# Performance work log

Hardware: AMD Instinct MI355X
Metric: run time of the kernel (lower is better)

## Reference

```python
import jax, jax.numpy as jnp
import numpy as np

B, N, H, E = 64, 512, 32, 4
N_STEPS = 5
ANNO = 1


def setup_inputs() -> dict:
    key = jax.random.key(0)
    ks = jax.random.split(key, 20)
    sc_h = 1.0 / np.sqrt(H)
    sc_3h = 1.0 / np.sqrt(3 * H)
    sc_ha = 1.0 / np.sqrt(H + ANNO)
    inp = {
        "x": jax.random.normal(ks[0], (B, N, H), jnp.float32),
        "a": jax.random.uniform(ks[1], (B, N, ANNO), jnp.float32),
        "m": jax.random.uniform(ks[2], (B, N, 2 * N * E), jnp.float32),
        # fc_in / fc_out: hidden -> hidden*n_edge (torch Linear: W [out,in])
        "W_in": jax.random.normal(ks[3], (H * E, H), jnp.float32) * sc_h,
        "b_in": jax.random.normal(ks[4], (H * E,), jnp.float32) * sc_h,
        "W_out": jax.random.normal(ks[5], (H * E, H), jnp.float32) * sc_h,
        "b_out": jax.random.normal(ks[6], (H * E,), jnp.float32) * sc_h,
        # GRU-style gates: 3*hidden -> hidden
        "Wz": jax.random.normal(ks[7], (H, 3 * H), jnp.float32) * sc_3h,
        "bz": jax.random.normal(ks[8], (H,), jnp.float32) * sc_3h,
        "Wr": jax.random.normal(ks[9], (H, 3 * H), jnp.float32) * sc_3h,
        "br": jax.random.normal(ks[10], (H,), jnp.float32) * sc_3h,
        "Wt": jax.random.normal(ks[11], (H, 3 * H), jnp.float32) * sc_3h,
        "bt": jax.random.normal(ks[12], (H,), jnp.float32) * sc_3h,
        # output head (task_id not in {18,19}): fc1, fc2
        "W1": jax.random.normal(ks[13], (H, H + ANNO), jnp.float32) * sc_ha,
        "b1": jax.random.normal(ks[14], (H,), jnp.float32) * sc_ha,
        "W2": jax.random.normal(ks[15], (1, H), jnp.float32) * sc_h,
        "b2": jax.random.normal(ks[16], (1,), jnp.float32) * sc_h,
    }
    return inp


def _reorder(s):
    # [B, N, H*E] -> view(B,N,H,E) -> transpose(2,3) -> transpose(1,2) -> [B, E*N, H]
    return s.reshape(B, N, H, E).transpose(0, 3, 1, 2).reshape(B, E * N, H)


def reference(x, a, m, W_in, b_in, W_out, b_out, Wz, bz, Wr, br, Wt, bt, W1, b1, W2, b2):
    m_in = m[:, :, : N * E]   # [B, N, N*E]
    m_out = m[:, :, N * E :]  # [B, N, N*E]
    h = x
    for _ in range(N_STEPS):
        s_in = _reorder(h @ W_in.T + b_in)    # [B, E*N, H]
        s_out = _reorder(h @ W_out.T + b_out)  # [B, E*N, H]
        a_in = jnp.einsum("bnm,bmh->bnh", m_in, s_in)
        a_out = jnp.einsum("bnm,bmh->bnh", m_out, s_out)
        cat = jnp.concatenate([a_in, a_out, h], axis=-1)  # [B, N, 3H]
        z = jax.nn.sigmoid(cat @ Wz.T + bz)
        r = jax.nn.sigmoid(cat @ Wr.T + br)
        joint = jnp.concatenate([a_in, a_out, r * h], axis=-1)
        h_hat = jnp.tanh(joint @ Wt.T + bt)
        h = (1.0 - z) * h + z * h_hat
    out = jnp.tanh(jnp.concatenate([h, a], axis=-1) @ W1.T + b1)  # [B, N, H]
    out = (out @ W2.T + b2).sum(-1)  # [B, N]
    return out
```

## Files before the change

kernel.cpp:

```cpp
#include <hip/hip_runtime.h>
#include <hip/hip_fp16.h>
#include <math.h>

#define B_ 64
#define N_ 512
#define H_ 32
#define E_ 4
#define NSTEPS 5
#define KTOT 2048

typedef _Float16 half8 __attribute__((ext_vector_type(8)));
typedef float   f32x4 __attribute__((ext_vector_type(4)));

__device__ __forceinline__ void gld16(const void* g, void* l) {
    __builtin_amdgcn_global_load_lds(
        (const __attribute__((address_space(1))) void*)g,
        (__attribute__((address_space(3))) void*)l, 16, 0, 0);
}

__global__ __launch_bounds__(256) void k_init_h(const float* __restrict__ x,
                                                float* __restrict__ h) {
    int i = blockIdx.x * blockDim.x + threadIdx.x;
    ((f32x4*)h)[i] = ((const f32x4*)x)[i];
}

__global__ __launch_bounds__(256) void k_s(const float* __restrict__ hstate,
                                           const float* __restrict__ W_in,
                                           const float* __restrict__ b_in,
                                           const float* __restrict__ W_out,
                                           const float* __restrict__ b_out,
                                           _Float16* __restrict__ sT_in_hi,
                                           _Float16* __restrict__ sT_in_lo,
                                           _Float16* __restrict__ sT_out_hi,
                                           _Float16* __restrict__ sT_out_lo) {
    int b  = blockIdx.x >> 3;
    int n0 = (blockIdx.x & 7) * 64;
    int lane = threadIdx.x & 63;
    int w = __builtin_amdgcn_readfirstlane((int)(threadIdx.x >> 6));
    int n = n0 + lane;

    const float* hrow = hstate + ((size_t)b * N_ + n) * H_;
    f32x4 hv[8];
#pragma unroll
    for (int c = 0; c < 8; c++) hv[c] = ((const f32x4*)hrow)[c];

#pragma unroll 4
    for (int o = 0; o < 32; o++) {
        int he = w * 32 + o;
        const f32x4* wr = (const f32x4*)(W_in + (size_t)he * H_);
        float acc = b_in[he];
#pragma unroll
        for (int c = 0; c < 8; c++) {
            f32x4 wv = wr[c];
            acc += hv[c][0]*wv[0] + hv[c][1]*wv[1] + hv[c][2]*wv[2] + hv[c][3]*wv[3];
        }
        int hh = he >> 2, e = he & 3;
        size_t idx = ((size_t)b * H_ + hh) * KTOT + e * N_ + n;
        _Float16 hi = (_Float16)acc;
        sT_in_hi[idx] = hi;
        sT_in_lo[idx] = (_Float16)(acc - (float)hi);
    }
#pragma unroll 4
    for (int o = 0; o < 32; o++) {
        int he = w * 32 + o;
        const f32x4* wr = (const f32x4*)(W_out + (size_t)he * H_);
        float acc = b_out[he];
#pragma unroll
        for (int c = 0; c < 8; c++) {
            f32x4 wv = wr[c];
            acc += hv[c][0]*wv[0] + hv[c][1]*wv[1] + hv[c][2]*wv[2] + hv[c][3]*wv[3];
        }
        int hh = he >> 2, e = he & 3;
        size_t idx = ((size_t)b * H_ + hh) * KTOT + e * N_ + n;
        _Float16 hi = (_Float16)acc;
        sT_out_hi[idx] = hi;
        sT_out_lo[idx] = (_Float16)(acc - (float)hi);
    }
}

#define CHB   256
#define BUFA2 16384
#define BUFB2 8192
#define BUFSZ 24576
#define NCH   32
__global__ __launch_bounds__(256, 2) void k_einsum_p3(const float* __restrict__ m,
                                                      const _Float16* __restrict__ sT_in_hi,
                                                      const _Float16* __restrict__ sT_in_lo,
                                                      const _Float16* __restrict__ sT_out_hi,
                                                      const _Float16* __restrict__ sT_out_lo,
                                                      float* __restrict__ a_in,
                                                      float* __restrict__ a_out) {
    __shared__ __align__(16) char lds[3 * BUFSZ];
    int bid  = blockIdx.x;
    int xcd  = bid & 7, loc = bid >> 3;
    int pair = xcd * 16 + (loc >> 3);
    int nblk = loc & 7;
    int b    = pair >> 1;
    int dir  = pair & 1;
    int n0   = nblk * 64;
    int tid  = threadIdx.x;
    int w    = tid >> 6;
    int lane = tid & 63;
    int l15  = lane & 15;
    int quad = lane >> 4;

    const char* mBase = (const char*)(m + ((size_t)(b * N_ + n0)) * (2 * KTOT)
                                        + (size_t)dir * KTOT);
    const _Float16* sHi = (dir ? sT_out_hi : sT_in_hi) + (size_t)b * H_ * KTOT;
    const _Float16* sLo = (dir ? sT_out_lo : sT_in_lo) + (size_t)b * H_ * KTOT;
    float* aout = dir ? a_out : a_in;

    int bp   = w >> 1;
    int brb  = (w & 1) << 4;
    const char* sP = (const char*)(bp ? sLo : sHi);

    auto STAGE = [&](int c, int buf) {
        char* dA = lds + buf * BUFSZ;
        char* dB = lds + buf * BUFSZ + BUFA2 + bp * 4096;
#pragma unroll
        for (int i = 0; i < 4; i++) {
            int r = (w << 4) + i * 4 + (lane >> 4);
            const char* g = mBase + (size_t)r * (2 * KTOT * 4) + c * CHB
                            + (((lane & 15) * 16) ^ ((r & 7) << 4));
            gld16(g, dA + ((w << 4) + i * 4) * 256);
        }
#pragma unroll
        for (int i = 0; i < 2; i++) {
            int r = brb + i * 8 + (lane >> 3);
            const char* g = sP + (size_t)r * (KTOT * 2) + c * 128
                            + (((lane & 7) * 16) ^ ((r & 7) << 4));
            gld16(g, dB + (brb + i * 8) * 128);
        }
    };

    f32x4 acc0 = {0.f,0.f,0.f,0.f}, acc1 = {0.f,0.f,0.f,0.f};

    int rowA  = (w << 4) + l15;
    int swzA  = (rowA & 7) << 4;
    int swzB0 = (l15 & 7) << 4;

    STAGE(0, 0);
    STAGE(1, 1);

    for (int c = 0; c < NCH; c++) {
        int buf = c % 3;
        if (c + 2 < NCH) STAGE(c + 2, (c + 2) % 3);
        if (c + 2 < NCH)      asm volatile("s_waitcnt vmcnt(12)" ::: "memory");
        else if (c + 1 < NCH) asm volatile("s_waitcnt vmcnt(6)"  ::: "memory");
        else                  asm volatile("s_waitcnt vmcnt(0)"  ::: "memory");
        __builtin_amdgcn_s_barrier();
        __builtin_amdgcn_sched_barrier(0);

        const char* Ab = lds + buf * BUFSZ + rowA * 256;
        const char* Bh = lds + buf * BUFSZ + BUFA2;
        const char* Bl = Bh + 4096;
#pragma unroll
        for (int it = 0; it < 2; it++) {
            int kab = it * 128 + quad * 32;
            f32x4 a0 = *(const f32x4*)(Ab + (kab ^ swzA));
            f32x4 a1 = *(const f32x4*)(Ab + ((kab + 16) ^ swzA));

            int kbb = it * 64 + quad * 16;
            int o0 = l15 * 128        + (kbb ^ swzB0);
            int o1 = (l15 + 16) * 128 + (kbb ^ swzB0);
            half8 Bhi0 = *(const half8*)(Bh + o0);
            half8 Bhi1 = *(const half8*)(Bh + o1);
            half8 Blo0 = *(const half8*)(Bl + o0);
            half8 Blo1 = *(const half8*)(Bl + o1);

            half8 Ahi, Alo;
#pragma unroll
            for (int j = 0; j < 4; j++) {
                float v0 = a0[j], v1 = a1[j];
                _Float16 h0 = (_Float16)v0, h1 = (_Float16)v1;
                Ahi[j]     = h0;
                Ahi[j + 4] = h1;
                Alo[j]     = (_Float16)(v0 - (float)h0);
                Alo[j + 4] = (_Float16)(v1 - (float)h1);
            }
            acc0 = __builtin_amdgcn_mfma_f32_16x16x32_f16(Ahi, Bhi0, acc0, 0, 0, 0);
            acc1 = __builtin_amdgcn_mfma_f32_16x16x32_f16(Ahi, Bhi1, acc1, 0, 0, 0);
            acc0 = __builtin_amdgcn_mfma_f32_16x16x32_f16(Ahi, Blo0, acc0, 0, 0, 0);
            acc1 = __builtin_amdgcn_mfma_f32_16x16x32_f16(Ahi, Blo1, acc1, 0, 0, 0);
            acc0 = __builtin_amdgcn_mfma_f32_16x16x32_f16(Alo, Bhi0, acc0, 0, 0, 0);
            acc1 = __builtin_amdgcn_mfma_f32_16x16x32_f16(Alo, Bhi1, acc1, 0, 0, 0);
        }
        __builtin_amdgcn_sched_barrier(0);
        __builtin_amdgcn_s_barrier();
    }

#pragma unroll
    for (int r = 0; r < 4; r++) {
        size_t rr = (size_t)b * N_ + (n0 + w * 16 + quad * 4 + r);
        aout[rr * H_ + l15]      = acc0[r];
        aout[rr * H_ + 16 + l15] = acc1[r];
    }
}

__global__ __launch_bounds__(256) void k_gate(const float* __restrict__ a_in,
                                              const float* __restrict__ a_out,
                                              float* __restrict__ hstate,
                                              const float* __restrict__ Wz,
                                              const float* __restrict__ bz,
                                              const float* __restrict__ Wr,
                                              const float* __restrict__ br,
                                              const float* __restrict__ Wt,
                                              const float* __restrict__ bt) {
    __shared__ float cat[8][96];
    __shared__ float rh[8][32];
    int base = blockIdx.x * 8;
    int t = threadIdx.x;

    for (int idx = t; idx < 768; idx += 256) {
        int r = idx / 96, c = idx - r * 96;
        size_t row = (size_t)(base + r);
        float v;
        if (c < 32)      v = a_in [row * 32 + c];
        else if (c < 64) v = a_out[row * 32 + (c - 32)];
        else             v = hstate[row * 32 + (c - 64)];
        cat[r][c] = v;
    }
    __syncthreads();

    int r = t >> 5, i = t & 31;
    float az = bz[i], ar = br[i];
    const f32x4* wzr = (const f32x4*)(Wz + (size_t)i * 96);
    const f32x4* wrr = (const f32x4*)(Wr + (size_t)i * 96);
    const f32x4* crow = (const f32x4*)cat[r];
#pragma unroll
    for (int kc = 0; kc < 24; kc++) {
        f32x4 cv = crow[kc];
        f32x4 wz = wzr[kc];
        f32x4 wr = wrr[kc];
        az += cv[0]*wz[0] + cv[1]*wz[1] + cv[2]*wz[2] + cv[3]*wz[3];
        ar += cv[0]*wr[0] + cv[1]*wr[1] + cv[2]*wr[2] + cv[3]*wr[3];
    }
    float z  = 1.f / (1.f + __expf(-az));
    float rg = 1.f / (1.f + __expf(-ar));
    float hold = cat[r][64 + i];
    rh[r][i] = rg * hold;
    __syncthreads();

    float at = bt[i];
    const f32x4* wtr = (const f32x4*)(Wt + (size_t)i * 96);
#pragma unroll
    for (int kc = 0; kc < 16; kc++) {
        f32x4 cv = crow[kc];
        f32x4 wt = wtr[kc];
        at += cv[0]*wt[0] + cv[1]*wt[1] + cv[2]*wt[2] + cv[3]*wt[3];
    }
    const f32x4* rrow = (const f32x4*)rh[r];
#pragma unroll
    for (int kc = 0; kc < 8; kc++) {
        f32x4 cv = rrow[kc];
        f32x4 wt = wtr[16 + kc];
        at += cv[0]*wt[0] + cv[1]*wt[1] + cv[2]*wt[2] + cv[3]*wt[3];
    }
    float hh = tanhf(at);
    hstate[(size_t)(base + r) * 32 + i] = (1.f - z) * hold + z * hh;
}

__global__ __launch_bounds__(256) void k_final(const float* __restrict__ hstate,
                                               const float* __restrict__ a,
                                               const float* __restrict__ W1,
                                               const float* __restrict__ b1,
                                               const float* __restrict__ W2,
                                               const float* __restrict__ b2,
                                               float* __restrict__ out) {
    __shared__ float hl[8][32];
    __shared__ float as[8];
    int base = blockIdx.x * 8;
    int t = threadIdx.x;
    {
        int r = t >> 5, c = t & 31;
        hl[r][c] = hstate[(size_t)(base + r) * 32 + c];
        if (t < 8) as[t] = a[base + t];
    }
    __syncthreads();
    int r = t >> 5, j = t & 31;
    float acc = b1[j];
    const float* w1r = W1 + (size_t)j * 33;
#pragma unroll
    for (int i2 = 0; i2 < 32; i2++) acc += hl[r][i2] * w1r[i2];
    acc += as[r] * w1r[32];
    float o = tanhf(acc) * W2[j];
#pragma unroll
    for (int off = 16; off; off >>= 1) o += __shfl_xor(o, off, 32);
    if (j == 0) out[base + r] = o + b2[0];
}

extern "C" void kernel_launch(void* const* d_in, const int* in_sizes, int n_in,
                              void* d_out, int out_size, void* d_ws, size_t ws_size,
                              hipStream_t stream) {
    const float* x     = (const float*)d_in[0];
    const float* a     = (const float*)d_in[1];
    const float* m     = (const float*)d_in[2];
    const float* W_in  = (const float*)d_in[3];
    const float* b_in  = (const float*)d_in[4];
    const float* W_out = (const float*)d_in[5];
    const float* b_out = (const float*)d_in[6];
    const float* Wz    = (const float*)d_in[7];
    const float* bz    = (const float*)d_in[8];
    const float* Wr    = (const float*)d_in[9];
    const float* br    = (const float*)d_in[10];
    const float* Wt    = (const float*)d_in[11];
    const float* bt    = (const float*)d_in[12];
    const float* W1    = (const float*)d_in[13];
    const float* b1    = (const float*)d_in[14];
    const float* W2    = (const float*)d_in[15];
    const float* b2    = (const float*)d_in[16];
    float* out = (float*)d_out;

    char* ws = (char*)d_ws;
    float*    h         = (float*)(ws);
    float*    a_in      = (float*)(ws + ((size_t)4  << 20));
    float*    a_out     = (float*)(ws + ((size_t)8  << 20));
    _Float16* sT_in_hi  = (_Float16*)(ws + ((size_t)12 << 20));
    _Float16* sT_in_lo  = (_Float16*)(ws + ((size_t)20 << 20));
    _Float16* sT_out_hi = (_Float16*)(ws + ((size_t)28 << 20));
    _Float16* sT_out_lo = (_Float16*)(ws + ((size_t)36 << 20));

    k_init_h<<<1024, 256, 0, stream>>>(x, h);
    for (int s = 0; s < NSTEPS; s++) {
        k_s<<<512, 256, 0, stream>>>(h, W_in, b_in, W_out, b_out,
                                     sT_in_hi, sT_in_lo, sT_out_hi, sT_out_lo);
        k_einsum_p3<<<1024, 256, 0, stream>>>(m, sT_in_hi, sT_in_lo,
                                              sT_out_hi, sT_out_lo,
                                              a_in, a_out);
        k_gate<<<4096, 256, 0, stream>>>(a_in, a_out, h, Wz, bz, Wr, br, Wt, bt);
    }
    k_final<<<4096, 256, 0, stream>>>(h, a, W1, b1, W2, b2, out);
}
```

Baseline: 2.176 ms.

## Fuse einsum and GRU gate into one kernel, drop init copy

Merges the two einsum directions and the gate computation into a single kernel. Each block handles both in and out directions for its 64 rows, keeping a_in/a_out in LDS instead of writing them to global memory. The initial h copy is removed by reading x directly on the first step. The grid halves from 1024 to 512 blocks, each doing twice the streaming work. Pipelining drops from triple to double buffering, which may expose more memory latency on the dominant m stream.

```diff
diff --git a/kernel.cpp b/kernel.cpp
--- a/kernel.cpp
+++ b/kernel.cpp
@@ -18,13 +18,7 @@
         (__attribute__((address_space(3))) void*)l, 16, 0, 0);
 }
 
-__global__ __launch_bounds__(256) void k_init_h(const float* __restrict__ x,
-                                                float* __restrict__ h) {
-    int i = blockIdx.x * blockDim.x + threadIdx.x;
-    ((f32x4*)h)[i] = ((const f32x4*)x)[i];
-}
-
-__global__ __launch_bounds__(256) void k_s(const float* __restrict__ hstate,
+__global__ __launch_bounds__(256) void k_s(const float* __restrict__ hsrc,
                                            const float* __restrict__ W_in,
                                            const float* __restrict__ b_in,
                                            const float* __restrict__ W_out,
@@ -39,7 +33,7 @@
     int w = __builtin_amdgcn_readfirstlane((int)(threadIdx.x >> 6));
     int n = n0 + lane;
 
-    const float* hrow = hstate + ((size_t)b * N_ + n) * H_;
+    const float* hrow = hsrc + ((size_t)b * N_ + n) * H_;
     f32x4 hv[8];
 #pragma unroll
     for (int c = 0; c < 8; c++) hv[c] = ((const f32x4*)hrow)[c];
@@ -80,23 +74,27 @@
 
 #define CHB   256
 #define BUFA2 16384
-#define BUFB2 8192
 #define BUFSZ 24576
-#define NCH   32
-__global__ __launch_bounds__(256, 2) void k_einsum_p3(const float* __restrict__ m,
-                                                      const _Float16* __restrict__ sT_in_hi,
-                                                      const _Float16* __restrict__ sT_in_lo,
-                                                      const _Float16* __restrict__ sT_out_hi,
-                                                      const _Float16* __restrict__ sT_out_lo,
-                                                      float* __restrict__ a_in,
-                                                      float* __restrict__ a_out) {
-    __shared__ __align__(16) char lds[3 * BUFSZ];
+__global__ __launch_bounds__(256, 2) void k_fuse(const float* __restrict__ m,
+                                                 const _Float16* __restrict__ sT_in_hi,
+                                                 const _Float16* __restrict__ sT_in_lo,
+                                                 const _Float16* __restrict__ sT_out_hi,
+                                                 const _Float16* __restrict__ sT_out_lo,
+                                                 const float* __restrict__ hold_src,
+                                                 float* __restrict__ hstate,
+                                                 const float* __restrict__ Wz,
+                                                 const float* __restrict__ bz,
+                                                 const float* __restrict__ Wr,
+                                                 const float* __restrict__ br,
+                                                 const float* __restrict__ Wt,
+                                                 const float* __restrict__ bt) {
+    __shared__ __align__(16) char lds[2 * BUFSZ];
+    __shared__ float aBuf[64][96];
+    __shared__ float rhL[8][32];
     int bid  = blockIdx.x;
     int xcd  = bid & 7, loc = bid >> 3;
-    int pair = xcd * 16 + (loc >> 3);
+    int b    = xcd * 8 + (loc >> 3);
     int nblk = loc & 7;
-    int b    = pair >> 1;
-    int dir  = pair & 1;
     int n0   = nblk * 64;
     int tid  = threadIdx.x;
     int w    = tid >> 6;
@@ -104,23 +102,29 @@
     int l15  = lane & 15;
     int quad = lane >> 4;
 
-    const char* mBase = (const char*)(m + ((size_t)(b * N_ + n0)) * (2 * KTOT)
-                                        + (size_t)dir * KTOT);
-    const _Float16* sHi = (dir ? sT_out_hi : sT_in_hi) + (size_t)b * H_ * KTOT;
-    const _Float16* sLo = (dir ? sT_out_lo : sT_in_lo) + (size_t)b * H_ * KTOT;
-    float* aout = dir ? a_out : a_in;
+    const char* mBase = (const char*)(m + ((size_t)(b * N_ + n0)) * (2 * KTOT));
+    const float* hold = hold_src + ((size_t)b * N_ + n0) * H_;
+
+    for (int i = tid; i < 2048; i += 256)
+        aBuf[i >> 5][64 + (i & 31)] = hold[((i >> 5) * 32) + (i & 31)];
 
     int bp   = w >> 1;
     int brb  = (w & 1) << 4;
-    const char* sP = (const char*)(bp ? sLo : sHi);
-
-    auto STAGE = [&](int c, int buf) {
+    const char* sHiD[2] = { (const char*)(sT_in_hi  + (size_t)b * H_ * KTOT),
+                            (const char*)(sT_out_hi + (size_t)b * H_ * KTOT) };
+    const char* sLoD[2] = { (const char*)(sT_in_lo  + (size_t)b * H_ * KTOT),
+                            (const char*)(sT_out_lo + (size_t)b * H_ * KTOT) };
+
+    auto STAGE = [&](int cc, int buf) {
+        int dir_s = cc >> 5, c = cc & 31;
         char* dA = lds + buf * BUFSZ;
         char* dB = lds + buf * BUFSZ + BUFA2 + bp * 4096;
+        const char* mD = mBase + dir_s * 8192;
+        const char* sP = bp ? sLoD[dir_s] : sHiD[dir_s];
 #pragma unroll
         for (int i = 0; i < 4; i++) {
             int r = (w << 4) + i * 4 + (lane >> 4);
-            const char* g = mBase + (size_t)r * (2 * KTOT * 4) + c * CHB
+            const char* g = mD + (size_t)r * (2 * KTOT * 4) + c * CHB
                             + (((lane & 15) * 16) ^ ((r & 7) << 4));
             gld16(g, dA + ((w << 4) + i * 4) * 256);
         }
@@ -140,14 +144,12 @@
     int swzB0 = (l15 & 7) << 4;
 
     STAGE(0, 0);
-    STAGE(1, 1);
-
-    for (int c = 0; c < NCH; c++) {
-        int buf = c % 3;
-        if (c + 2 < NCH) STAGE(c + 2, (c + 2) % 3);
-        if (c + 2 < NCH)      asm volatile("s_waitcnt vmcnt(12)" ::: "memory");
-        else if (c + 1 < NCH) asm volatile("s_waitcnt vmcnt(6)"  ::: "memory");
-        else                  asm volatile("s_waitcnt vmcnt(0)"  ::: "memory");
+
+    for (int cc = 0; cc < 64; cc++) {
+        int buf = cc & 1;
+        if (cc < 63) STAGE(cc + 1, buf ^ 1);
+        if (cc < 63) asm volatile("s_waitcnt vmcnt(6)" ::: "memory");
+        else         asm volatile("s_waitcnt vmcnt(0)" ::: "memory");
         __builtin_amdgcn_s_barrier();
         __builtin_amdgcn_sched_barrier(0);
 
@@ -185,79 +187,69 @@
             acc0 = __builtin_amdgcn_mfma_f32_16x16x32_f16(Alo, Bhi0, acc0, 0, 0, 0);
             acc1 = __builtin_amdgcn_mfma_f32_16x16x32_f16(Alo, Bhi1, acc1, 0, 0, 0);
         }
+        if (cc == 31) {
+            int row = (w << 4) + (quad << 2);
+#pragma unroll
+            for (int r = 0; r < 4; r++) {
+                aBuf[row + r][l15]      = acc0[r];
+                aBuf[row + r][16 + l15] = acc1[r];
+            }
+            acc0 = (f32x4){0.f,0.f,0.f,0.f};
+            acc1 = (f32x4){0.f,0.f,0.f,0.f};
+        }
         __builtin_amdgcn_sched_barrier(0);
         __builtin_amdgcn_s_barrier();
     }
-
-#pragma unroll
-    for (int r = 0; r < 4; r++) {
-        size_t rr = (size_t)b * N_ + (n0 + w * 16 + quad * 4 + r);
-        aout[rr * H_ + l15]      = acc0[r];
-        aout[rr * H_ + 16 + l15] = acc1[r];
-    }
-}
-
-__global__ __launch_bounds__(256) void k_gate(const float* __restrict__ a_in,
-                                              const float* __restrict__ a_out,
-                                              float* __restrict__ hstate,
-                                              const float* __restrict__ Wz,
-                                              const float* __restrict__ bz,
-                                              const float* __restrict__ Wr,
-                                              const float* __restrict__ br,
-                                              const float* __restrict__ Wt,
-                                              const float* __restrict__ bt) {
-    __shared__ float cat[8][96];
-    __shared__ float rh[8][32];
-    int base = blockIdx.x * 8;
-    int t = threadIdx.x;
-
-    for (int idx = t; idx < 768; idx += 256) {
-        int r = idx / 96, c = idx - r * 96;
-        size_t row = (size_t)(base + r);
-        float v;
-        if (c < 32)      v = a_in [row * 32 + c];
-        else if (c < 64) v = a_out[row * 32 + (c - 32)];
-        else             v = hstate[row * 32 + (c - 64)];
-        cat[r][c] = v;
+    {
+        int row = (w << 4) + (quad << 2);
+#pragma unroll
+        for (int r = 0; r < 4; r++) {
+            aBuf[row + r][32 + l15] = acc0[r];
+            aBuf[row + r][48 + l15] = acc1[r];
+        }
     }
     __syncthreads();
 
-    int r = t >> 5, i = t & 31;
-    float az = bz[i], ar = br[i];
-    const f32x4* wzr = (const f32x4*)(Wz + (size_t)i * 96);
-    const f32x4* wrr = (const f32x4*)(Wr + (size_t)i * 96);
-    const f32x4* crow = (const f32x4*)cat[r];
-#pragma unroll
-    for (int kc = 0; kc < 24; kc++) {
-        f32x4 cv = crow[kc];
-        f32x4 wz = wzr[kc];
-        f32x4 wr = wrr[kc];
-        az += cv[0]*wz[0] + cv[1]*wz[1] + cv[2]*wz[2] + cv[3]*wz[3];
-        ar += cv[0]*wr[0] + cv[1]*wr[1] + cv[2]*wr[2] + cv[3]*wr[3];
-    }
-    float z  = 1.f / (1.f + __expf(-az));
-    float rg = 1.f / (1.f + __expf(-ar));
-    float hold = cat[r][64 + i];
-    rh[r][i] = rg * hold;
-    __syncthreads();
-
-    float at = bt[i];
-    const f32x4* wtr = (const f32x4*)(Wt + (size_t)i * 96);
-#pragma unroll
-    for (int kc = 0; kc < 16; kc++) {
-        f32x4 cv = crow[kc];
-        f32x4 wt = wtr[kc];
-        at += cv[0]*wt[0] + cv[1]*wt[1] + cv[2]*wt[2] + cv[3]*wt[3];
-    }
-    const f32x4* rrow = (const f32x4*)rh[r];
-#pragma unroll
-    for (int kc = 0; kc < 8; kc++) {
-        f32x4 cv = rrow[kc];
-        f32x4 wt = wtr[16 + kc];
-        at += cv[0]*wt[0] + cv[1]*wt[1] + cv[2]*wt[2] + cv[3]*wt[3];
-    }
-    float hh = tanhf(at);
-    hstate[(size_t)(base + r) * 32 + i] = (1.f - z) * hold + z * hh;
+    int rg = tid >> 5, ig = tid & 31;
+    for (int ps = 0; ps < 8; ps++) {
+        int row = ps * 8 + rg;
+        float az = bz[ig], ar = br[ig];
+        const f32x4* wzr = (const f32x4*)(Wz + (size_t)ig * 96);
+        const f32x4* wrr = (const f32x4*)(Wr + (size_t)ig * 96);
+        const f32x4* crow = (const f32x4*)aBuf[row];
+#pragma unroll
+        for (int kc = 0; kc < 24; kc++) {
+            f32x4 cv = crow[kc];
+            f32x4 wz = wzr[kc];
+            f32x4 wr = wrr[kc];
+            az += cv[0]*wz[0] + cv[1]*wz[1] + cv[2]*wz[2] + cv[3]*wz[3];
+            ar += cv[0]*wr[0] + cv[1]*wr[1] + cv[2]*wr[2] + cv[3]*wr[3];
+        }
+        float z  = 1.f / (1.f + __expf(-az));
+        float rgt = 1.f / (1.f + __expf(-ar));
+        float holdv = aBuf[row][64 + ig];
+        rhL[rg][ig] = rgt * holdv;
+        __syncthreads();
+
+        float at = bt[ig];
+        const f32x4* wtr = (const f32x4*)(Wt + (size_t)ig * 96);
+#pragma unroll
+        for (int kc = 0; kc < 16; kc++) {
+            f32x4 cv = crow[kc];
+            f32x4 wt = wtr[kc];
+            at += cv[0]*wt[0] + cv[1]*wt[1] + cv[2]*wt[2] + cv[3]*wt[3];
+        }
+        const f32x4* rrow = (const f32x4*)rhL[rg];
+#pragma unroll
+        for (int kc = 0; kc < 8; kc++) {
+            f32x4 cv = rrow[kc];
+            f32x4 wt = wtr[16 + kc];
+            at += cv[0]*wt[0] + cv[1]*wt[1] + cv[2]*wt[2] + cv[3]*wt[3];
+        }
+        float hh = tanhf(at);
+        hstate[((size_t)b * N_ + n0 + row) * H_ + ig] = (1.f - z) * holdv + z * hh;
+        __syncthreads();
+    }
 }
 
 __global__ __launch_bounds__(256) void k_final(const float* __restrict__ hstate,
@@ -313,21 +305,18 @@
 
     char* ws = (char*)d_ws;
     float*    h         = (float*)(ws);
-    float*    a_in      = (float*)(ws + ((size_t)4  << 20));
-    float*    a_out     = (float*)(ws + ((size_t)8  << 20));
-    _Float16* sT_in_hi  = (_Float16*)(ws + ((size_t)12 << 20));
-    _Float16* sT_in_lo  = (_Float16*)(ws + ((size_t)20 << 20));
-    _Float16* sT_out_hi = (_Float16*)(ws + ((size_t)28 << 20));
-    _Float16* sT_out_lo = (_Float16*)(ws + ((size_t)36 << 20));
-
-    k_init_h<<<1024, 256, 0, stream>>>(x, h);
+    _Float16* sT_in_hi  = (_Float16*)(ws + ((size_t)4  << 20));
+    _Float16* sT_in_lo  = (_Float16*)(ws + ((size_t)12 << 20));
+    _Float16* sT_out_hi = (_Float16*)(ws + ((size_t)20 << 20));
+    _Float16* sT_out_lo = (_Float16*)(ws + ((size_t)28 << 20));
+
     for (int s = 0; s < NSTEPS; s++) {
-        k_s<<<512, 256, 0, stream>>>(h, W_in, b_in, W_out, b_out,
+        const float* hsrc = (s == 0) ? x : h;
+        k_s<<<512, 256, 0, stream>>>(hsrc, W_in, b_in, W_out, b_out,
                                      sT_in_hi, sT_in_lo, sT_out_hi, sT_out_lo);
-        k_einsum_p3<<<1024, 256, 0, stream>>>(m, sT_in_hi, sT_in_lo,
-                                              sT_out_hi, sT_out_lo,
-                                              a_in, a_out);
-        k_gate<<<4096, 256, 0, stream>>>(a_in, a_out, h, Wz, bz, Wr, br, Wt, bt);
+        k_fuse<<<512, 256, 0, stream>>>(m, sT_in_hi, sT_in_lo,
+                                        sT_out_hi, sT_out_lo,
+                                        hsrc, h, Wz, bz, Wr, br, Wt, bt);
     }
     k_final<<<4096, 256, 0, stream>>>(h, a, W1, b1, W2, b2, out);
 }
```

Measured after the change: 2.392 ms. +9.9%, slower.

## Pre-pack adjacency matrix into swizzled tile-contiguous layout reused across steps

Applied to the files above, without the earlier changes.

Adds a one-time kernel that repacks m into per-tile contiguous, pre-swizzled chunks, so each einsum step loads A tiles with fully coalesced contiguous 16-byte loads. The new einsum kernel uses double buffering instead of triple buffering and has no occupancy hint. It also removes the init copy of x by reading x directly in the first step. The repack costs one extra full pass over m (512MB read plus write) per call and needs a large workspace; if the workspace is smaller, the old path runs.

```diff
diff --git a/kernel.cpp b/kernel.cpp
--- a/kernel.cpp
+++ b/kernel.cpp
@@ -18,13 +18,7 @@
         (__attribute__((address_space(3))) void*)l, 16, 0, 0);
 }
 
-__global__ __launch_bounds__(256) void k_init_h(const float* __restrict__ x,
-                                                float* __restrict__ h) {
-    int i = blockIdx.x * blockDim.x + threadIdx.x;
-    ((f32x4*)h)[i] = ((const f32x4*)x)[i];
-}
-
-__global__ __launch_bounds__(256) void k_s(const float* __restrict__ hstate,
+__global__ __launch_bounds__(256) void k_s(const float* __restrict__ hsrc,
                                            const float* __restrict__ W_in,
                                            const float* __restrict__ b_in,
                                            const float* __restrict__ W_out,
@@ -39,7 +33,7 @@
     int w = __builtin_amdgcn_readfirstlane((int)(threadIdx.x >> 6));
     int n = n0 + lane;
 
-    const float* hrow = hstate + ((size_t)b * N_ + n) * H_;
+    const float* hrow = hsrc + ((size_t)b * N_ + n) * H_;
     f32x4 hv[8];
 #pragma unroll
     for (int c = 0; c < 8; c++) hv[c] = ((const f32x4*)hrow)[c];
@@ -78,11 +72,133 @@
     }
 }
 
-#define CHB   256
+__global__ __launch_bounds__(256) void k_packm(const float* __restrict__ m,
+                                               char* __restrict__ pm) {
+    int tile = blockIdx.x;
+    int b = tile >> 4, dir = (tile >> 3) & 1, nblk = tile & 7;
+    const char* src = (const char*)m
+        + ((size_t)(b * N_ + nblk * 64)) * (2 * KTOT * 4) + dir * (KTOT * 4);
+    char* dst = pm + (size_t)tile * 524288;
+    int tid = threadIdx.x;
+    for (int i = tid; i < 32768; i += 256) {
+        int r = i >> 9, sg = i & 511;
+        f32x4 v = *(const f32x4*)(src + (size_t)r * 16384 + sg * 16);
+        int c = sg >> 4, s2 = sg & 15;
+        *(f32x4*)(dst + (size_t)(c * 64 + r) * 256
+                      + ((s2 * 16) ^ ((r & 7) << 4))) = v;
+    }
+}
+
 #define BUFA2 16384
-#define BUFB2 8192
 #define BUFSZ 24576
-#define NCH   32
+__global__ __launch_bounds__(256) void k_einsum_pk(const char* __restrict__ pm,
+                                                   const _Float16* __restrict__ sT_in_hi,
+                                                   const _Float16* __restrict__ sT_in_lo,
+                                                   const _Float16* __restrict__ sT_out_hi,
+                                                   const _Float16* __restrict__ sT_out_lo,
+                                                   float* __restrict__ a_in,
+                                                   float* __restrict__ a_out) {
+    __shared__ __align__(16) char lds[2 * BUFSZ];
+    int nblk = blockIdx.x;
+    int b    = blockIdx.y;
+    int dir  = blockIdx.z;
+    int n0   = nblk * 64;
+    int tid  = threadIdx.x;
+    int w    = tid >> 6;
+    int lane = tid & 63;
+    int l15  = lane & 15;
+    int quad = lane >> 4;
+
+    const char* pmT = pm + (size_t)((b * 2 + dir) * 8 + nblk) * 524288;
+    const char* sHi = (const char*)((dir ? sT_out_hi : sT_in_hi) + (size_t)b * H_ * KTOT);
+    const char* sLo = (const char*)((dir ? sT_out_lo : sT_in_lo) + (size_t)b * H_ * KTOT);
+    float* aout = dir ? a_out : a_in;
+
+    int bp  = w >> 1;
+    int brb = (w & 1) << 4;
+    const char* sP = bp ? sLo : sHi;
+
+    auto STAGE = [&](int c, int buf) {
+        char* dA = lds + buf * BUFSZ;
+        char* dB = lds + buf * BUFSZ + BUFA2 + bp * 4096;
+        const char* gA = pmT + (size_t)c * 16384;
+#pragma unroll
+        for (int i = 0; i < 4; i++) {
+            int off = ((w << 4) + i * 4) * 256;
+            gld16(gA + off + lane * 16, dA + off);
+        }
+#pragma unroll
+        for (int i = 0; i < 2; i++) {
+            int r = brb + i * 8 + (lane >> 3);
+            const char* g = sP + (size_t)r * (KTOT * 2) + c * 128
+                            + (((lane & 7) * 16) ^ ((r & 7) << 4));
+            gld16(g, dB + (brb + i * 8) * 128);
+        }
+    };
+
+    f32x4 acc0 = {0.f,0.f,0.f,0.f}, acc1 = {0.f,0.f,0.f,0.f};
+
+    int rowA  = (w << 4) + l15;
+    int swzA  = (rowA & 7) << 4;
+    int swzB0 = (l15 & 7) << 4;
+
+    STAGE(0, 0);
+
+    for (int c = 0; c < 32; c++) {
+        int buf = c & 1;
+        if (c < 31) STAGE(c + 1, buf ^ 1);
+        if (c < 31) asm volatile("s_waitcnt vmcnt(6)" ::: "memory");
+        else        asm volatile("s_waitcnt vmcnt(0)" ::: "memory");
+        __builtin_amdgcn_s_barrier();
+        __builtin_amdgcn_sched_barrier(0);
+
+        const char* Ab = lds + buf * BUFSZ + rowA * 256;
+        const char* Bh = lds + buf * BUFSZ + BUFA2;
+        const char* Bl = Bh + 4096;
+#pragma unroll
+        for (int it = 0; it < 2; it++) {
+            int kab = it * 128 + quad * 32;
+            f32x4 a0 = *(const f32x4*)(Ab + (kab ^ swzA));
+            f32x4 a1 = *(const f32x4*)(Ab + ((kab + 16) ^ swzA));
+
+            int kbb = it * 64 + quad * 16;
+            int o0 = l15 * 128        + (kbb ^ swzB0);
+            int o1 = (l15 + 16) * 128 + (kbb ^ swzB0);
+            half8 Bhi0 = *(const half8*)(Bh + o0);
+            half8 Bhi1 = *(const half8*)(Bh + o1);
+            half8 Blo0 = *(const half8*)(Bl + o0);
+            half8 Blo1 = *(const half8*)(Bl + o1);
+
+            half8 Ahi, Alo;
+#pragma unroll
+            for (int j = 0; j < 4; j++) {
+                float v0 = a0[j], v1 = a1[j];
+                _Float16 h0 = (_Float16)v0, h1 = (_Float16)v1;
+                Ahi[j]     = h0;
+                Ahi[j + 4] = h1;
+                Alo[j]     = (_Float16)(v0 - (float)h0);
+                Alo[j + 4] = (_Float16)(v1 - (float)h1);
+            }
+            acc0 = __builtin_amdgcn_mfma_f32_16x16x32_f16(Ahi, Bhi0, acc0, 0, 0, 0);
+            acc1 = __builtin_amdgcn_mfma_f32_16x16x32_f16(Ahi, Bhi1, acc1, 0, 0, 0);
+            acc0 = __builtin_amdgcn_mfma_f32_16x16x32_f16(Ahi, Blo0, acc0, 0, 0, 0);
+            acc1 = __builtin_amdgcn_mfma_f32_16x16x32_f16(Ahi, Blo1, acc1, 0, 0, 0);
+            acc0 = __builtin_amdgcn_mfma_f32_16x16x32_f16(Alo, Bhi0, acc0, 0, 0, 0);
+            acc1 = __builtin_amdgcn_mfma_f32_16x16x32_f16(Alo, Bhi1, acc1, 0, 0, 0);
+        }
+        __builtin_amdgcn_sched_barrier(0);
+        __builtin_amdgcn_s_barrier();
+    }
+
+#pragma unroll
+    for (int r = 0; r < 4; r++) {
+        size_t rr = (size_t)b * N_ + (n0 + w * 16 + quad * 4 + r);
+        aout[rr * H_ + l15]      = acc0[r];
+        aout[rr * H_ + 16 + l15] = acc1[r];
+    }
+}
+
+#define CHB 256
 __global__ __launch_bounds__(256, 2) void k_einsum_p3(const float* __restrict__ m,
                                                       const _Float16* __restrict__ sT_in_hi,
                                                       const _Float16* __restrict__ sT_in_lo,
@@ -134,20 +250,18 @@
     };
 
     f32x4 acc0 = {0.f,0.f,0.f,0.f}, acc1 = {0.f,0.f,0.f,0.f};
-
     int rowA  = (w << 4) + l15;
     int swzA  = (rowA & 7) << 4;
     int swzB0 = (l15 & 7) << 4;
 
     STAGE(0, 0);
     STAGE(1, 1);
-
-    for (int c = 0; c < NCH; c++) {
+    for (int c = 0; c < 32; c++) {
         int buf = c % 3;
-        if (c + 2 < NCH) STAGE(c + 2, (c + 2) % 3);
-        if (c + 2 < NCH)      asm volatile("s_waitcnt vmcnt(12)" ::: "memory");
-        else if (c + 1 < NCH) asm volatile("s_waitcnt vmcnt(6)"  ::: "memory");
-        else                  asm volatile("s_waitcnt vmcnt(0)"  ::: "memory");
+        if (c + 2 < 32) STAGE(c + 2, (c + 2) % 3);
+        if (c + 2 < 32)      asm volatile("s_waitcnt vmcnt(12)" ::: "memory");
+        else if (c + 1 < 32) asm volatile("s_waitcnt vmcnt(6)"  ::: "memory");
+        else                 asm volatile("s_waitcnt vmcnt(0)"  ::: "memory");
         __builtin_amdgcn_s_barrier();
         __builtin_amdgcn_sched_barrier(0);
 
@@ -159,7 +273,6 @@
             int kab = it * 128 + quad * 32;
             f32x4 a0 = *(const f32x4*)(Ab + (kab ^ swzA));
             f32x4 a1 = *(const f32x4*)(Ab + ((kab + 16) ^ swzA));
-
             int kbb = it * 64 + quad * 16;
             int o0 = l15 * 128        + (kbb ^ swzB0);
             int o1 = (l15 + 16) * 128 + (kbb ^ swzB0);
@@ -167,15 +280,13 @@
             half8 Bhi1 = *(const half8*)(Bh + o1);
             half8 Blo0 = *(const half8*)(Bl + o0);
             half8 Blo1 = *(const half8*)(Bl + o1);
-
             half8 Ahi, Alo;
 #pragma unroll
             for (int j = 0; j < 4; j++) {
                 float v0 = a0[j], v1 = a1[j];
                 _Float16 h0 = (_Float16)v0, h1 = (_Float16)v1;
-                Ahi[j]     = h0;
-                Ahi[j + 4] = h1;
-                Alo[j]     = (_Float16)(v0 - (float)h0);
+                Ahi[j] = h0; Ahi[j + 4] = h1;
+                Alo[j] = (_Float16)(v0 - (float)h0);
                 Alo[j + 4] = (_Float16)(v1 - (float)h1);
             }
             acc0 = __builtin_amdgcn_mfma_f32_16x16x32_f16(Ahi, Bhi0, acc0, 0, 0, 0);
@@ -188,7 +299,6 @@
         __builtin_amdgcn_sched_barrier(0);
         __builtin_amdgcn_s_barrier();
     }
-
 #pragma unroll
     for (int r = 0; r < 4; r++) {
         size_t rr = (size_t)b * N_ + (n0 + w * 16 + quad * 4 + r);
@@ -199,6 +309,7 @@
 
 __global__ __launch_bounds__(256) void k_gate(const float* __restrict__ a_in,
                                               const float* __restrict__ a_out,
+                                              const float* __restrict__ hold_src,
                                               float* __restrict__ hstate,
                                               const float* __restrict__ Wz,
                                               const float* __restrict__ bz,
@@ -217,7 +328,7 @@
         float v;
         if (c < 32)      v = a_in [row * 32 + c];
         else if (c < 64) v = a_out[row * 32 + (c - 32)];
-        else             v = hstate[row * 32 + (c - 64)];
+        else             v = hold_src[row * 32 + (c - 64)];
         cat[r][c] = v;
     }
     __syncthreads();
@@ -319,15 +430,27 @@
     _Float16* sT_in_lo  = (_Float16*)(ws + ((size_t)20 << 20));
     _Float16* sT_out_hi = (_Float16*)(ws + ((size_t)28 << 20));
     _Float16* sT_out_lo = (_Float16*)(ws + ((size_t)36 << 20));
-
-    k_init_h<<<1024, 256, 0, stream>>>(x, h);
+    char*     pm        = ws + ((size_t)48 << 20);
+
+    const int use_pack = (ws_size >= ((size_t)560 << 20));
+
+    if (use_pack)
+        k_packm<<<1024, 256, 0, stream>>>(m, pm);
+
     for (int s = 0; s < NSTEPS; s++) {
-        k_s<<<512, 256, 0, stream>>>(h, W_in, b_in, W_out, b_out,
+        const float* hsrc = (s == 0) ? x : h;
+        k_s<<<512, 256, 0, stream>>>(hsrc, W_in, b_in, W_out, b_out,
                                      sT_in_hi, sT_in_lo, sT_out_hi, sT_out_lo);
-        k_einsum_p3<<<1024, 256, 0, stream>>>(m, sT_in_hi, sT_in_lo,
-                                              sT_out_hi, sT_out_lo,
-                                              a_in, a_out);
-        k_gate<<<4096, 256, 0, stream>>>(a_in, a_out, h, Wz, bz, Wr, br, Wt, bt);
+        if (use_pack)
+            k_einsum_pk<<<dim3(8, 64, 2), 256, 0, stream>>>(pm, sT_in_hi, sT_in_lo,
+                                                            sT_out_hi, sT_out_lo,
+                                                            a_in, a_out);
+        else
+            k_einsum_p3<<<1024, 256, 0, stream>>>(m, sT_in_hi, sT_in_lo,
+                                                  sT_out_hi, sT_out_lo,
+                                                  a_in, a_out);
+        k_gate<<<4096, 256, 0, stream>>>(a_in, a_out, hsrc, h,
+                                         Wz, bz, Wr, br, Wt, bt);
     }
     k_final<<<4096, 256, 0, stream>>>(h, a, W1, b1, W2, b2, out);
 }
```

Result: slower. 2.388 ms (+9.7%).
